# Performance work log

Measured on AMD Instinct MI355X. Metric: run time of the kernel, lower is better.

## Reference

```python
import jax, jax.numpy as jnp
import numpy as np

N = 50000      # nodes
E = 600000     # edges
D_IN = 128
D = 128        # embedding_size
H = 2 * D      # GENConv MLP hidden (expansion=2, num_layers=2)
L = 6          # gnn_layers
OUT = 2        # out_channels
EPS_MSG = 1e-7   # GENConv message eps
EPS_SM = 1e-16   # PyG softmax denominator eps
LN_EPS = 1e-5


def setup_inputs() -> dict:
    key = jax.random.key(0)
    ks = jax.random.split(key, 18)
    s_in = 1.0 / np.sqrt(D_IN)
    s_d = 1.0 / np.sqrt(D)
    s_h = 1.0 / np.sqrt(H)
    return {
        "x": jax.random.normal(ks[0], (N, D_IN), jnp.float32),
        "edge_index": jax.random.randint(ks[1], (2, E), 0, N, jnp.int64),
        # node encoder
        "enc_W": jax.random.normal(ks[2], (D_IN, D), jnp.float32) * s_in,
        "enc_b": jnp.zeros((D,), jnp.float32),
        # per-layer DeepGCN params (stacked over L layers)
        "ln_g": jnp.ones((L, D), jnp.float32),
        "ln_b": jnp.zeros((L, D), jnp.float32),
        "t": jnp.ones((L,), jnp.float32),  # learnable softmax temperature
        "W1": jax.random.normal(ks[3], (L, D, H), jnp.float32) * s_d,
        "b1": jnp.zeros((L, H), jnp.float32),
        "mln_g": jnp.ones((L, H), jnp.float32),
        "mln_b": jnp.zeros((L, H), jnp.float32),
        "W2": jax.random.normal(ks[4], (L, H, D), jnp.float32) * s_h,
        "b2": jnp.zeros((L, D), jnp.float32),
        # final MLP head (linear_layers=2)
        "lin_W1": jax.random.normal(ks[5], (D, D), jnp.float32) * s_d,
        "lin_b1": jnp.zeros((D,), jnp.float32),
        "lin_W2": jax.random.normal(ks[6], (D, OUT), jnp.float32) * s_d,
        "lin_b2": jnp.zeros((OUT,), jnp.float32),
    }


def _layernorm(h, g, b):
    mu = jnp.mean(h, axis=-1, keepdims=True)
    var = jnp.mean(jnp.square(h - mu), axis=-1, keepdims=True)
    return (h - mu) * jax.lax.rsqrt(var + LN_EPS) * g + b


def _genconv(h, src, dst, t, W1, b1, mg, mb, W2, b2):
    """GENConv with softmax aggregation: gather -> segment softmax -> scatter -> MLP."""
    msg = jax.nn.relu(h[src]) + EPS_MSG            # [E, D]
    scaled = msg * t
    mmax = jax.ops.segment_max(scaled, dst, num_segments=N)  # [N, D]
    mmax = jnp.where(jnp.isfinite(mmax), mmax, 0.0)          # empty segments
    ex = jnp.exp(scaled - mmax[dst])                          # [E, D]
    denom = jax.ops.segment_sum(ex, dst, num_segments=N)     # [N, D]
    alpha = ex / (denom[dst] + EPS_SM)
    agg = jax.ops.segment_sum(msg * alpha, dst, num_segments=N)  # [N, D]
    out = agg + h                                  # root/self term
    z = out @ W1 + b1                              # [N, 2D]
    z = jax.nn.relu(_layernorm(z, mg, mb))
    return z @ W2 + b2                             # [N, D]


def reference(x, edge_index, enc_W, enc_b, ln_g, ln_b, t, W1, b1,
              mln_g, mln_b, W2, b2, lin_W1, lin_b1, lin_W2, lin_b2):
    src, dst = edge_index[0], edge_index[1]
    h = x @ enc_W + enc_b                          # node encoder [N, D]
    for i in range(L):                             # DeepGCNLayer 'res+' blocks
        g = _layernorm(h, ln_g[i], ln_b[i])
        g = jax.nn.relu(g)                         # (dropout: inference no-op)
        g = _genconv(g, src, dst, t[i], W1[i], b1[i], mln_g[i], mln_b[i], W2[i], b2[i])
        h = h + g
    h = jax.nn.relu(h @ lin_W1 + lin_b1)           # head (dropout_rate=None)
    return h @ lin_W2 + lin_b2                     # [N, OUT]
```

## Files before the change

kernel.cpp:

```cpp
#include <hip/hip_runtime.h>

#define NN 50000
#define EE 600000
#define DD 128
#define HH 256
#define LL 6
#define NB 49

typedef _Float16 f16x8 __attribute__((ext_vector_type(8)));
typedef float f32x4 __attribute__((ext_vector_type(4)));

__device__ __forceinline__ float bf2f(unsigned short u){
  unsigned int x = ((unsigned int)u) << 16; float f; __builtin_memcpy(&f, &x, 4); return f;
}
__device__ __forceinline__ unsigned short f2bf(float f){
  unsigned int x; __builtin_memcpy(&x, &f, 4);
  unsigned int lsb = (x >> 16) & 1u; x += 0x7fffu + lsb; return (unsigned short)(x >> 16);
}
__device__ __forceinline__ float wave_sum(float v){
  #pragma unroll
  for (int off = 32; off >= 1; off >>= 1) v += __shfl_xor(v, off, 64);
  return v;
}
__device__ __forceinline__ unsigned short f2h(float f){
  _Float16 h = (_Float16)f; unsigned short u; __builtin_memcpy(&u, &h, 2); return u;
}
__device__ __forceinline__ float h2f(unsigned short u){
  _Float16 h; __builtin_memcpy(&h, &u, 2); return (float)h;
}

__global__ void k_detect(const unsigned short* __restrict__ xh,
                         const unsigned int* __restrict__ ew,
                         int* __restrict__ flags){
  __shared__ int s_bad, s_nz;
  int t = threadIdx.x;
  if (t == 0){ s_bad = 0; s_nz = 0; }
  __syncthreads();
  int bad = 0;
  for (int i = t; i < 512; i += 256){
    unsigned e = (xh[i] >> 7) & 0xffu;
    if (e < 96u || e > 135u) bad = 1;
  }
  if (bad) atomicOr(&s_bad, 1);
  int nz = 0;
  for (int i = t; i < 1024; i += 256)
    if ((i & 1) && ew[i] != 0u) nz = 1;
  if (nz) atomicOr(&s_nz, 1);
  __syncthreads();
  if (t == 0){
    flags[0] = s_bad ? 1 : 0;
    flags[1] = s_nz ? 0 : 1;
  }
}

__global__ void k_cvt_edges(const void* __restrict__ ei, const int* __restrict__ flags,
                            int* __restrict__ s32, int* __restrict__ d32){
  int e = blockIdx.x*256 + threadIdx.x;
  if (e >= EE) return;
  int sv, dv;
  if (flags[1]){
    const long long* p = (const long long*)ei;
    sv = (int)p[e]; dv = (int)p[EE + e];
  } else {
    const int* p = (const int*)ei;
    sv = p[e]; dv = p[EE + e];
  }
  s32[e] = ((unsigned)sv < (unsigned)NN) ? sv : 0;
  d32[e] = ((unsigned)dv < (unsigned)NN) ? dv : 0;
}

__global__ void k_hist(const int* __restrict__ dst, int* __restrict__ deg){
  int e = blockIdx.x*256 + threadIdx.x;
  if (e < EE) atomicAdd(&deg[dst[e]], 1);
}

__global__ void k_blocksum(const int* __restrict__ deg, int* __restrict__ bsum){
  __shared__ int ws[4];
  int t = threadIdx.x, b = blockIdx.x;
  int s = 0;
  int i0 = b*1024 + t*4;
  #pragma unroll
  for (int j=0;j<4;j++){ int i = i0+j; if (i < NN) s += deg[i]; }
  #pragma unroll
  for (int off=32; off>=1; off>>=1) s += __shfl_xor(s, off, 64);
  if ((t&63)==0) ws[t>>6] = s;
  __syncthreads();
  if (t==0) bsum[b] = ws[0]+ws[1]+ws[2]+ws[3];
}

__global__ void k_scanb(const int* __restrict__ bsum, int* __restrict__ boff, int* __restrict__ rowptr){
  int lane = threadIdx.x;
  int v = (lane < NB) ? bsum[lane] : 0;
  int inc = v;
  #pragma unroll
  for (int off=1; off<64; off<<=1){ int u = __shfl_up(inc, off, 64); if (lane>=off) inc += u; }
  if (lane < NB) boff[lane] = inc - v;
  if (lane == 63) rowptr[NN] = inc;
}

__global__ void k_scanscatter(const int* __restrict__ deg, const int* __restrict__ boff,
                              int* __restrict__ rowptr, int* __restrict__ pos){
  __shared__ int ws[4];
  int t = threadIdx.x, b = blockIdx.x;
  int lane = t & 63, wid = t >> 6;
  int i0 = b*1024 + t*4;
  int d[4];
  #pragma unroll
  for (int j=0;j<4;j++){ int i=i0+j; d[j] = (i<NN)? deg[i] : 0; }
  int tot = d[0]+d[1]+d[2]+d[3];
  int inc = tot;
  #pragma unroll
  for (int off=1; off<64; off<<=1){ int u = __shfl_up(inc, off, 64); if (lane>=off) inc += u; }
  if (lane==63) ws[wid] = inc;
  __syncthreads();
  int woff = 0;
  for (int w=0; w<wid; w++) woff += ws[w];
  int base = boff[b] + woff + (inc - tot);
  int pre = 0;
  #pragma unroll
  for (int j=0;j<4;j++){
    int i = i0+j;
    if (i<NN){ rowptr[i] = base + pre; pos[i] = base + pre; }
    pre += d[j];
  }
}

__global__ void k_fill(const int* __restrict__ src, const int* __restrict__ dst,
                       int* __restrict__ pos, int* __restrict__ csr){
  int e = blockIdx.x*256 + threadIdx.x;
  if (e < EE){
    int d = dst[e];
    int p = atomicAdd(&pos[d], 1);
    csr[p] = src[e];
  }
}

__global__ void k_prep_w(const int* __restrict__ flags,
    const void* __restrict__ encW, const void* __restrict__ linW1,
    const void* __restrict__ W1, const void* __restrict__ W2,
    unsigned short* __restrict__ ph, unsigned short* __restrict__ pl)
{
  int idx = blockIdx.x*256 + threadIdx.x;
  int fp32 = flags[0];
  const void* src; int off;
  if (idx < 16384){ int n=idx>>7, k=idx&127; src=encW; off=k*128+n; }
  else if (idx < 32768){ int o=idx-16384; int n=o>>7, k=o&127; src=linW1; off=k*128+n; }
  else if (idx < 229376){ int o=idx-32768; int l=o>>15, r=o&32767; int n=r>>7, k=r&127; src=W1; off=l*32768+k*256+n; }
  else { int o=idx-229376; int l=o>>15, r=o&32767; int n=r>>8, k=r&255; src=W2; off=l*32768+k*128+n; }
  float w = fp32 ? ((const float*)src)[off] : bf2f(((const unsigned short*)src)[off]);
  unsigned short h = f2h(w);
  ph[idx] = h;
  pl[idx] = f2h(w - h2f(h));
}

#define SM_ENCB 0
#define SM_LNG 128
#define SM_LNB 896
#define SM_TV 1664
#define SM_B1 1670
#define SM_MG 3206
#define SM_MB 4742
#define SM_B2 6278
#define SM_LINB1 7046
#define SM_LINW2 7174
#define SM_LINB2 7430
#define SM_TOT 7432
__global__ void k_prep_small(const int* __restrict__ flags,
    const void* s0, const void* s1, const void* s2, const void* s3,
    const void* s4, const void* s5, const void* s6, const void* s7,
    const void* s8, const void* s9, const void* s10, float* __restrict__ out)
{
  int i = blockIdx.x*256 + threadIdx.x;
  if (i >= SM_TOT) return;
  int fp32 = flags[0];
  const void* src; int off;
  if      (i < SM_LNG)  { src=s0;  off=i; }
  else if (i < SM_LNB)  { src=s1;  off=i-SM_LNG; }
  else if (i < SM_TV)   { src=s2;  off=i-SM_LNB; }
  else if (i < SM_B1)   { src=s3;  off=i-SM_TV; }
  else if (i < SM_MG)   { src=s4;  off=i-SM_B1; }
  else if (i < SM_MB)   { src=s5;  off=i-SM_MG; }
  else if (i < SM_B2)   { src=s6;  off=i-SM_MB; }
  else if (i < SM_LINB1){ src=s7;  off=i-SM_B2; }
  else if (i < SM_LINW2){ src=s8;  off=i-SM_LINB1; }
  else if (i < SM_LINB2){ src=s9;  off=i-SM_LINW2; }
  else                  { src=s10; off=i-SM_LINB2; }
  out[i] = fp32 ? ((const float*)src)[off] : bf2f(((const unsigned short*)src)[off]);
}

__device__ __forceinline__ void emit_me(unsigned short* me, int row, int col, float g, float tv){
  float m = g + 1e-7f;
  me[(size_t)row*256 + col] = f2h(m);
  me[(size_t)row*256 + 128 + col] = f2h(__expf(fminf(m*tv, 18.f) - 8.f));
}

template<int EPI>
__global__ __launch_bounds__(256, 4) void k_gemm(const void* __restrict__ Ap,
    const unsigned short* __restrict__ WTh, const unsigned short* __restrict__ WTl,
    const float* __restrict__ bias, void* __restrict__ Cv,
    int M, const int* __restrict__ flags, int aExt)
{
  __shared__ __align__(16) char smem[27648];
  short* lA = (short*)smem;
  short* lW = (short*)(smem + 9216);
  short* hT = (short*)smem;

  const int tid = threadIdx.x, lane = tid & 63, wid = tid >> 6;
  const int mi = lane & 15, q = lane >> 4;
  const int rowb = blockIdx.x * 64;
  const int fp32m = flags[0];

  f32x4 acc[4][2];
  #pragma unroll
  for (int a=0;a<4;a++)
    #pragma unroll
    for (int c=0;c<2;c++){ acc[a][c][0]=0.f; acc[a][c][1]=0.f; acc[a][c][2]=0.f; acc[a][c][3]=0.f; }

  const int nW = fp32m ? 2 : 1;
  for (int pass = 0; pass < nW; ++pass){
    const unsigned short* Wp = pass ? WTl : WTh;
    for (int kc = 0; kc < 2; ++kc){
      {
        const int kv = (tid & 7) * 8, r0 = tid >> 3;
        #pragma unroll
        for (int p = 0; p < 2; ++p){
          int row = p*32 + r0, grow = rowb + row;
          uint4 d = make_uint4(0u,0u,0u,0u);
          if (grow < M){
            if (!aExt){
              d = *(const uint4*)((const unsigned short*)Ap + (size_t)grow*128 + kc*64 + kv);
            } else if (!fp32m){
              uint4 u = *(const uint4*)((const unsigned short*)Ap + (size_t)grow*128 + kc*64 + kv);
              const unsigned short* us = (const unsigned short*)&u;
              unsigned short hh[8];
              #pragma unroll
              for (int c=0;c<8;c++) hh[c] = f2h(bf2f(us[c]));
              d.x = hh[0]|((unsigned)hh[1]<<16); d.y = hh[2]|((unsigned)hh[3]<<16);
              d.z = hh[4]|((unsigned)hh[5]<<16); d.w = hh[6]|((unsigned)hh[7]<<16);
            } else {
              const float* fp = (const float*)Ap + (size_t)grow*128 + kc*64 + kv;
              float4 v0 = *(const float4*)fp, v1 = *(const float4*)(fp+4);
              unsigned short hh[8] = {f2h(v0.x),f2h(v0.y),f2h(v0.z),f2h(v0.w),
                                      f2h(v1.x),f2h(v1.y),f2h(v1.z),f2h(v1.w)};
              d.x = hh[0]|((unsigned)hh[1]<<16); d.y = hh[2]|((unsigned)hh[3]<<16);
              d.z = hh[4]|((unsigned)hh[5]<<16); d.w = hh[6]|((unsigned)hh[7]<<16);
            }
          }
          *(uint4*)&lA[row*72 + kv] = d;
        }
        #pragma unroll
        for (int p = 0; p < 4; ++p){
          int n = p*32 + (tid >> 3);
          *(uint4*)&lW[n*72 + (tid & 7)*8] = *(const uint4*)(Wp + (size_t)n*128 + kc*64 + (tid & 7)*8);
        }
      }
      __syncthreads();
      #pragma unroll
      for (int ks = 0; ks < 2; ++ks){
        const int koff = ks*32 + q*8;
        f16x8 af[4], bw[2];
        #pragma unroll
        for (int rt=0; rt<4; rt++) af[rt] = *(const f16x8*)&lA[(rt*16+mi)*72 + koff];
        #pragma unroll
        for (int ct=0; ct<2; ct++) bw[ct] = *(const f16x8*)&lW[(wid*32 + ct*16 + mi)*72 + koff];
        #pragma unroll
        for (int rt=0; rt<4; rt++)
          #pragma unroll
          for (int ct=0; ct<2; ct++)
            acc[rt][ct] = __builtin_amdgcn_mfma_f32_16x16x32_f16(af[rt], bw[ct], acc[rt][ct], 0,0,0);
      }
      __syncthreads();
    }
  }
  #pragma unroll
  for (int ct=0; ct<2; ct++){
    const int col = wid*32 + ct*16 + mi;
    const float bf = bias[col];
    #pragma unroll
    for (int rt=0; rt<4; rt++)
      #pragma unroll
      for (int r=0; r<4; r++){
        float v = acc[rt][ct][r] + bf;
        if (EPI == 4) v = fmaxf(v, 0.f);
        hT[(rt*16 + q*4 + r)*136 + col] = (short)f2h(v);
      }
  }
  __syncthreads();
  unsigned short* C16 = (unsigned short*)Cv;
  #pragma unroll
  for (int i = 0; i < 4; ++i){
    int idx = i*256 + tid;
    int prow = idx >> 4, pl = idx & 15;
    int grow = rowb + prow;
    if (grow < M)
      *(uint4*)(C16 + (size_t)grow*128 + pl*8) = *(const uint4*)&hT[prow*136 + pl*8];
  }
}

__global__ __launch_bounds__(256, 3) void k_layer(const unsigned short* __restrict__ Ap,
    const unsigned short* __restrict__ W1h, const unsigned short* __restrict__ W1l,
    const unsigned short* __restrict__ W2h, const unsigned short* __restrict__ W2l,
    const float* __restrict__ b1, const float* __restrict__ mg, const float* __restrict__ mb,
    const float* __restrict__ b2, unsigned short* __restrict__ h16,
    const float* __restrict__ gam, const float* __restrict__ bet,
    const float* __restrict__ tp, unsigned short* __restrict__ me,
    int M, const int* __restrict__ flags, int doLN)
{
  __shared__ __align__(16) char smem[53248];
  short* lA  = (short*)smem;
  short* lW1 = (short*)(smem + 9216);
  short* zT  = (short*)smem;
  short* lW2 = (short*)(smem + 33792);
  short* hT  = (short*)smem;
  short* mE  = (short*)(smem + 17408);
  float2* sred = (float2*)(smem + 51200);

  const int tid = threadIdx.x, lane = tid & 63, wid = tid >> 6;
  const int mi = lane & 15, q = lane >> 4;
  const int kv = (tid & 7) * 8, r0 = tid >> 3;
  const int rowb = blockIdx.x * 64;
  const float tv = tp[0];
  const int nW = flags[0] ? 2 : 1;
  const int prow = tid >> 4;
  const int pl = tid & 15;

  f32x4 acc1[4][4];
  #pragma unroll
  for (int a=0;a<4;a++)
    #pragma unroll
    for (int c=0;c<4;c++){ acc1[a][c][0]=0.f; acc1[a][c][1]=0.f; acc1[a][c][2]=0.f; acc1[a][c][3]=0.f; }

  for (int pass = 0; pass < nW; ++pass){
    const unsigned short* Wp = pass ? W1l : W1h;
    for (int kc = 0; kc < 2; ++kc){
      if (pass == 0){
        #pragma unroll
        for (int p = 0; p < 2; ++p){
          int row = p*32 + r0, grow = rowb + row;
          uint4 d = make_uint4(0u,0u,0u,0u);
          if (grow < M) d = *(const uint4*)(Ap + (size_t)grow*128 + kc*64 + kv);
          *(uint4*)&lA[row*72 + kv] = d;
        }
      }
      #pragma unroll
      for (int p = 0; p < 8; ++p){
        int n = p*32 + r0;
        *(uint4*)&lW1[n*72 + kv] = *(const uint4*)(Wp + (size_t)n*128 + kc*64 + kv);
      }
      __syncthreads();
      #pragma unroll
      for (int ks = 0; ks < 2; ++ks){
        const int koff = ks*32 + q*8;
        f16x8 af[4], bw[4];
        #pragma unroll
        for (int rt=0; rt<4; rt++) af[rt] = *(const f16x8*)&lA[(rt*16+mi)*72 + koff];
        #pragma unroll
        for (int ct=0; ct<4; ct++) bw[ct] = *(const f16x8*)&lW1[(wid*64 + ct*16 + mi)*72 + koff];
        #pragma unroll
        for (int rt=0; rt<4; rt++)
          #pragma unroll
          for (int ct=0; ct<4; ct++)
            acc1[rt][ct] = __builtin_amdgcn_mfma_f32_16x16x32_f16(af[rt], bw[ct], acc1[rt][ct], 0,0,0);
      }
      __syncthreads();
    }
  }
  #pragma unroll
  for (int ct=0; ct<4; ct++){
    const float bf = b1[wid*64 + ct*16 + mi];
    #pragma unroll
    for (int rt=0; rt<4; rt++)
      #pragma unroll
      for (int r=0; r<4; r++) acc1[rt][ct][r] += bf;
  }
  #pragma unroll
  for (int rt=0; rt<4; rt++)
    #pragma unroll
    for (int r=0; r<4; r++){
      float s = 0.f, s2 = 0.f;
      #pragma unroll
      for (int ct=0; ct<4; ct++){ float v = acc1[rt][ct][r]; s += v; s2 += v*v; }
      #pragma unroll
      for (int off=1; off<16; off<<=1){ s += __shfl_xor(s, off, 64); s2 += __shfl_xor(s2, off, 64); }
      if (mi == 0) sred[wid*64 + rt*16 + q*4 + r] = make_float2(s, s2);
    }
  __syncthreads();
  float lnm[4][4], lnr[4][4];
  #pragma unroll
  for (int rt=0; rt<4; rt++)
    #pragma unroll
    for (int r=0; r<4; r++){
      int rl = rt*16 + q*4 + r;
      float2 t0 = sred[0*64+rl], t1 = sred[1*64+rl], t2 = sred[2*64+rl], t3 = sred[3*64+rl];
      float s = t0.x + t1.x + t2.x + t3.x;
      float s2 = t0.y + t1.y + t2.y + t3.y;
      float m = s * (1.f/256.f);
      float var = s2 * (1.f/256.f) - m*m;
      lnm[rt][r] = m;
      lnr[rt][r] = rsqrtf(var + 1e-5f);
    }
  __syncthreads();
  #pragma unroll
  for (int ct=0; ct<4; ct++){
    const int col = wid*64 + ct*16 + mi;
    const float gc = mg[col], bc = mb[col];
    #pragma unroll
    for (int rt=0; rt<4; rt++)
      #pragma unroll
      for (int r=0; r<4; r++){
        int rl = rt*16 + q*4 + r;
        float v = (acc1[rt][ct][r] - lnm[rt][r]) * lnr[rt][r] * gc + bc;
        zT[rl*264 + col] = (short)f2h(fmaxf(v, 0.f));
      }
  }
  __syncthreads();
  uint4 hpre[4];
  #pragma unroll
  for (int i = 0; i < 4; ++i){
    int grow = rowb + i*16 + prow;
    hpre[i] = make_uint4(0u,0u,0u,0u);
    if (grow < M) hpre[i] = *(const uint4*)(h16 + (size_t)grow*128 + pl*8);
  }
  f32x4 acc2[4][2];
  #pragma unroll
  for (int a=0;a<4;a++)
    #pragma unroll
    for (int c=0;c<2;c++){ acc2[a][c][0]=0.f; acc2[a][c][1]=0.f; acc2[a][c][2]=0.f; acc2[a][c][3]=0.f; }

  for (int pass = 0; pass < nW; ++pass){
    const unsigned short* Wp = pass ? W2l : W2h;
    for (int kc = 0; kc < 4; ++kc){
      #pragma unroll
      for (int p = 0; p < 4; ++p){
        int n = p*32 + r0;
        *(uint4*)&lW2[n*72 + kv] = *(const uint4*)(Wp + (size_t)n*256 + kc*64 + kv);
      }
      __syncthreads();
      #pragma unroll
      for (int ks = 0; ks < 2; ++ks){
        const int koff = ks*32 + q*8;
        f16x8 af[4], bw[2];
        #pragma unroll
        for (int rt=0; rt<4; rt++) af[rt] = *(const f16x8*)&zT[(rt*16+mi)*264 + kc*64 + koff];
        #pragma unroll
        for (int ct=0; ct<2; ct++) bw[ct] = *(const f16x8*)&lW2[(wid*32 + ct*16 + mi)*72 + koff];
        #pragma unroll
        for (int rt=0; rt<4; rt++)
          #pragma unroll
          for (int ct=0; ct<2; ct++)
            acc2[rt][ct] = __builtin_amdgcn_mfma_f32_16x16x32_f16(af[rt], bw[ct], acc2[rt][ct], 0,0,0);
      }
      __syncthreads();
    }
  }
  #pragma unroll
  for (int i = 0; i < 4; ++i)
    *(uint4*)&hT[(i*16 + prow)*136 + pl*8] = hpre[i];
  __syncthreads();
  #pragma unroll
  for (int ct=0; ct<2; ct++){
    const int col = wid*32 + ct*16 + mi;
    const float bf = b2[col];
    #pragma unroll
    for (int rt=0; rt<4; rt++)
      #pragma unroll
      for (int r=0; r<4; r++){
        int rl = rt*16 + q*4 + r;
        float hv = acc2[rt][ct][r] + bf + h2f((unsigned short)hT[rl*136 + col]);
        hT[rl*136 + col] = (short)f2h(hv);
        acc2[rt][ct][r] = hv;
      }
  }
  if (doLN){
    #pragma unroll
    for (int rt=0; rt<4; rt++)
      #pragma unroll
      for (int r=0; r<4; r++){
        float s = 0.f, s2 = 0.f;
        #pragma unroll
        for (int ct=0; ct<2; ct++){ float v = acc2[rt][ct][r]; s += v; s2 += v*v; }
        #pragma unroll
        for (int off=1; off<16; off<<=1){ s += __shfl_xor(s, off, 64); s2 += __shfl_xor(s2, off, 64); }
        if (mi == 0) sred[wid*64 + rt*16 + q*4 + r] = make_float2(s, s2);
      }
    __syncthreads();
    #pragma unroll
    for (int rt=0; rt<4; rt++)
      #pragma unroll
      for (int r=0; r<4; r++){
        int rl = rt*16 + q*4 + r;
        float2 t0 = sred[0*64+rl], t1 = sred[1*64+rl], t2 = sred[2*64+rl], t3 = sred[3*64+rl];
        float s = t0.x + t1.x + t2.x + t3.x;
        float s2 = t0.y + t1.y + t2.y + t3.y;
        float m = s * (1.f/128.f);
        float var = s2 * (1.f/128.f) - m*m;
        float rs = rsqrtf(var + 1e-5f);
        #pragma unroll
        for (int ct=0; ct<2; ct++){
          int col = wid*32 + ct*16 + mi;
          float g = fmaxf((acc2[rt][ct][r] - m) * rs * gam[col] + bet[col], 0.f);
          float mm = g + 1e-7f;
          mE[rl*264 + col] = (short)f2h(mm);
          mE[rl*264 + 128 + col] = (short)f2h(__expf(fminf(mm*tv, 18.f) - 8.f));
        }
      }
  }
  __syncthreads();
  #pragma unroll
  for (int i = 0; i < 4; ++i){
    int grow = rowb + i*16 + prow;
    if (grow < M)
      *(uint4*)(h16 + (size_t)grow*128 + pl*8) = *(const uint4*)&hT[(i*16 + prow)*136 + pl*8];
  }
  if (doLN){
    #pragma unroll
    for (int i = 0; i < 8; ++i){
      int idx2 = i*256 + tid;
      int mrow = idx2 >> 5, part = (idx2 >> 4) & 1, l16 = idx2 & 15;
      int grow = rowb + mrow;
      if (grow < M)
        *(uint4*)(me + (size_t)grow*256 + part*128 + l16*8)
          = *(const uint4*)&mE[mrow*264 + part*128 + l16*8];
    }
  }
}

__global__ __launch_bounds__(256,4) void k_preln0(const unsigned short* __restrict__ h16,
    const float* __restrict__ gam, const float* __restrict__ bet,
    const float* __restrict__ tp, unsigned short* __restrict__ me)
{
  int wid = threadIdx.x >> 6, lane = threadIdx.x & 63;
  int row = blockIdx.x*4 + wid;
  float tv = tp[0];
  unsigned u = ((const unsigned*)(h16 + (size_t)row*DD))[lane];
  float v0 = h2f((unsigned short)(u & 0xffffu));
  float v1 = h2f((unsigned short)(u >> 16));
  float mean = wave_sum(v0+v1) * (1.f/128.f);
  float d0 = v0-mean, d1 = v1-mean;
  float var = wave_sum(d0*d0 + d1*d1) * (1.f/128.f);
  float rs = rsqrtf(var + 1e-5f);
  float o0 = fmaxf(d0*rs*gam[2*lane]   + bet[2*lane],   0.f);
  float o1 = fmaxf(d1*rs*gam[2*lane+1] + bet[2*lane+1], 0.f);
  emit_me(me, row, 2*lane,   o0, tv);
  emit_me(me, row, 2*lane+1, o1, tv);
}

__global__ __launch_bounds__(256,8) void k_agg(
    const unsigned short* __restrict__ me,
    const int* __restrict__ rowptr, const int* __restrict__ csr,
    unsigned short* __restrict__ obf)
{
  int wid = threadIdx.x>>6, lane = threadIdx.x&63;
  int node = blockIdx.x*4 + wid;
  int st = rowptr[node], en = rowptr[node+1];
  int quad = lane >> 4, fi = lane & 15;
  float l[8], ac[8];
  #pragma unroll
  for (int f=0; f<8; f++){ l[f]=0.f; ac[f]=0.f; }
  for (int base = st; base < en; base += 64){
    int cnt = min(64, en - base);
    int sv = (lane < cnt) ? csr[base + lane] : NN;
    for (int j = 0; j < cnt; j += 8){
      int s0i = __shfl(sv, j + quad, 64);
      int s1i = __shfl(sv, j + 4 + quad, 64);
      bool two = (j + 4) < cnt;
      const unsigned short* mer0 = me + (size_t)s0i*256 + fi*8;
      f16x8 mh0 = *(const f16x8*)(mer0);
      f16x8 eh0 = *(const f16x8*)(mer0 + 128);
      if (two){
        const unsigned short* mer1 = me + (size_t)s1i*256 + fi*8;
        f16x8 mh1 = *(const f16x8*)(mer1);
        f16x8 eh1 = *(const f16x8*)(mer1 + 128);
        #pragma unroll
        for (int f=0; f<8; f++){
          l[f]  = fmaf((float)eh0[f], 1.f, l[f]);
          ac[f] = fmaf((float)mh0[f], (float)eh0[f], ac[f]);
          l[f]  = fmaf((float)eh1[f], 1.f, l[f]);
          ac[f] = fmaf((float)mh1[f], (float)eh1[f], ac[f]);
        }
      } else {
        #pragma unroll
        for (int f=0; f<8; f++){
          l[f]  = fmaf((float)eh0[f], 1.f, l[f]);
          ac[f] = fmaf((float)mh0[f], (float)eh0[f], ac[f]);
        }
      }
    }
  }
  #pragma unroll
  for (int off=16; off<=32; off<<=1)
    #pragma unroll
    for (int f=0; f<8; f++){ l[f] += __shfl_xor(l[f], off, 64); ac[f] += __shfl_xor(ac[f], off, 64); }
  if (quad == 0){
    f16x8 mh = *(const f16x8*)(me + (size_t)node*256 + fi*8);
    unsigned short o[8];
    #pragma unroll
    for (int f=0; f<8; f++){
      float a = ac[f] / (l[f] + 1e-16f);
      o[f] = f2h(((float)mh[f] - 1e-7f) + a);
    }
    uint4 w;
    w.x = o[0]|((unsigned)o[1]<<16); w.y = o[2]|((unsigned)o[3]<<16);
    w.z = o[4]|((unsigned)o[5]<<16); w.w = o[6]|((unsigned)o[7]<<16);
    *(uint4*)(obf + (size_t)node*DD + fi*8) = w;
  }
}

__global__ __launch_bounds__(256,4) void k_head2(const unsigned short* __restrict__ u16,
    const float* __restrict__ w, const float* __restrict__ b,
    void* __restrict__ out, const int* __restrict__ flags)
{
  int wid = threadIdx.x>>6, lane = threadIdx.x&63;
  int row = blockIdx.x*4 + wid;
  unsigned uu = ((const unsigned*)(u16 + (size_t)row*DD))[lane];
  float u0 = h2f((unsigned short)(uu & 0xffffu));
  float u1 = h2f((unsigned short)(uu >> 16));
  float s0 = u0*w[(2*lane)*2+0] + u1*w[(2*lane+1)*2+0];
  float s1 = u0*w[(2*lane)*2+1] + u1*w[(2*lane+1)*2+1];
  s0 = wave_sum(s0); s1 = wave_sum(s1);
  if (lane == 0){
    float o0 = s0 + b[0], o1 = s1 + b[1];
    if (flags[0]){
      ((float*)out)[row*2+0] = o0;
      ((float*)out)[row*2+1] = o1;
    } else {
      ((unsigned short*)out)[row*2+0] = f2bf(o0);
      ((unsigned short*)out)[row*2+1] = f2bf(o1);
    }
  }
}

extern "C" void kernel_launch(void* const* d_in, const int* in_sizes, int n_in,
                              void* d_out, int out_size, void* d_ws, size_t ws_size,
                              hipStream_t stream)
{
  (void)in_sizes; (void)n_in; (void)out_size; (void)ws_size;
  char* ws = (char*)d_ws;
  size_t off = 0;
  auto alloc = [&](size_t bytes) -> char* {
    char* p = ws + off;
    off = (off + bytes + 255) & ~(size_t)255;
    return p;
  };
  int* flags  = (int*)alloc(256);
  float* sm   = (float*)alloc(SM_TOT*4);
  unsigned short* planeH = (unsigned short*)alloc(425984*2);
  unsigned short* planeL = (unsigned short*)alloc(425984*2);
  int* src32  = (int*)alloc((size_t)EE*4);
  int* dst32  = (int*)alloc((size_t)EE*4);
  int* deg    = (int*)alloc((size_t)NN*4);
  int* pos    = (int*)alloc((size_t)NN*4);
  int* rowptr = (int*)alloc((size_t)(NN+1)*4);
  int* csr    = (int*)alloc((size_t)EE*4);
  int* bsum   = (int*)alloc(64*4);
  int* boff   = (int*)alloc(64*4);
  unsigned short* h16 = (unsigned short*)alloc((size_t)NN*128*2);
  unsigned short* me   = (unsigned short*)alloc((size_t)(NN+1)*256*2);
  unsigned short* obf  = (unsigned short*)alloc((size_t)NN*128*2);
  unsigned short* ob16 = (unsigned short*)alloc((size_t)NN*128*2);

  k_detect<<<1,256,0,stream>>>((const unsigned short*)d_in[0], (const unsigned int*)d_in[1], flags);
  k_cvt_edges<<<(EE+255)/256,256,0,stream>>>(d_in[1], flags, src32, dst32);
  hipMemsetAsync(deg, 0, (size_t)NN*4, stream);
  hipMemsetAsync(me + (size_t)NN*256, 0, 512, stream);
  k_hist<<<(EE+255)/256,256,0,stream>>>(dst32, deg);
  k_blocksum<<<NB,256,0,stream>>>(deg, bsum);
  k_scanb<<<1,64,0,stream>>>(bsum, boff, rowptr);
  k_scanscatter<<<NB,256,0,stream>>>(deg, boff, rowptr, pos);
  k_fill<<<(EE+255)/256,256,0,stream>>>(src32, dst32, pos, csr);
  k_prep_w<<<1664,256,0,stream>>>(flags, d_in[2], d_in[13], d_in[7], d_in[11], planeH, planeL);
  k_prep_small<<<30,256,0,stream>>>(flags, d_in[3], d_in[4], d_in[5], d_in[6], d_in[8],
                                    d_in[9], d_in[10], d_in[12], d_in[14], d_in[15], d_in[16], sm);

  const int GB = (NN + 63)/64;
  k_gemm<3><<<GB,256,0,stream>>>((const void*)d_in[0], planeH + 0, planeL + 0,
                                 sm + SM_ENCB, (void*)h16, NN, flags, 1);
  k_preln0<<<NN/4,256,0,stream>>>(h16, sm + SM_LNG, sm + SM_LNB, sm + SM_TV, me);
  for (int i = 0; i < LL; ++i){
    k_agg<<<NN/4,256,0,stream>>>(me, rowptr, csr, obf);
    int nl = (i+1 < LL) ? (i+1) : 0;
    k_layer<<<GB,256,0,stream>>>(obf,
                                 planeH + 32768 + i*32768, planeL + 32768 + i*32768,
                                 planeH + 229376 + i*32768, planeL + 229376 + i*32768,
                                 sm + SM_B1 + i*256, sm + SM_MG + i*256, sm + SM_MB + i*256,
                                 sm + SM_B2 + i*128, h16,
                                 sm + SM_LNG + nl*128, sm + SM_LNB + nl*128,
                                 sm + SM_TV + nl,
                                 me, NN, flags, (i+1 < LL) ? 1 : 0);
  }
  k_gemm<4><<<GB,256,0,stream>>>((const void*)h16, planeH + 16384, planeL + 16384,
                                 sm + SM_LINB1, (void*)ob16, NN, flags, 0);
  k_head2<<<NN/4,256,0,stream>>>(ob16, sm + SM_LINW2, sm + SM_LINB2, d_out, flags);
}
```

Before: 812.7 us.

## Register-prefetch next K-tile in layer GEMMs and fuse edge conversion with degree histogram

The per-layer fused MLP kernel now loads the next A/W1 and W2 K-chunks into registers while MFMAs run on the current LDS tile, so global-load latency is hidden behind compute. It also prefetches the first W2 chunk during the LayerNorm epilogue and adjusts barrier placement. Separately, edge index conversion and the degree histogram atomics are merged into one kernel, removing a launch and a reread of dst. Extra prefetch registers may raise VGPR pressure and reduce occupancy.

```diff
diff --git a/kernel.cpp b/kernel.cpp
--- a/kernel.cpp
+++ b/kernel.cpp
@@ -53,8 +53,9 @@
   }
 }
 
-__global__ void k_cvt_edges(const void* __restrict__ ei, const int* __restrict__ flags,
-                            int* __restrict__ s32, int* __restrict__ d32){
+__global__ void k_cvt_hist(const void* __restrict__ ei, const int* __restrict__ flags,
+                           int* __restrict__ s32, int* __restrict__ d32,
+                           int* __restrict__ deg){
   int e = blockIdx.x*256 + threadIdx.x;
   if (e >= EE) return;
   int sv, dv;
@@ -65,13 +66,11 @@
     const int* p = (const int*)ei;
     sv = p[e]; dv = p[EE + e];
   }
-  s32[e] = ((unsigned)sv < (unsigned)NN) ? sv : 0;
-  d32[e] = ((unsigned)dv < (unsigned)NN) ? dv : 0;
-}
-
-__global__ void k_hist(const int* __restrict__ dst, int* __restrict__ deg){
-  int e = blockIdx.x*256 + threadIdx.x;
-  if (e < EE) atomicAdd(&deg[dst[e]], 1);
+  sv = ((unsigned)sv < (unsigned)NN) ? sv : 0;
+  dv = ((unsigned)dv < (unsigned)NN) ? dv : 0;
+  s32[e] = sv;
+  d32[e] = dv;
+  atomicAdd(&deg[dv], 1);
 }
 
 __global__ void k_blocksum(const int* __restrict__ deg, int* __restrict__ bsum){
@@ -323,6 +322,7 @@
   const int nW = flags[0] ? 2 : 1;
   const int prow = tid >> 4;
   const int pl = tid & 15;
+  const int grow0 = rowb + r0, grow1 = rowb + 32 + r0;
 
   f32x4 acc1[4][4];
   #pragma unroll
@@ -330,41 +330,53 @@
     #pragma unroll
     for (int c=0;c<4;c++){ acc1[a][c][0]=0.f; acc1[a][c][1]=0.f; acc1[a][c][2]=0.f; acc1[a][c][3]=0.f; }
 
-  for (int pass = 0; pass < nW; ++pass){
-    const unsigned short* Wp = pass ? W1l : W1h;
-    for (int kc = 0; kc < 2; ++kc){
-      if (pass == 0){
-        #pragma unroll
-        for (int p = 0; p < 2; ++p){
-          int row = p*32 + r0, grow = rowb + row;
-          uint4 d = make_uint4(0u,0u,0u,0u);
-          if (grow < M) d = *(const uint4*)(Ap + (size_t)grow*128 + kc*64 + kv);
-          *(uint4*)&lA[row*72 + kv] = d;
-        }
-      }
-      #pragma unroll
-      for (int p = 0; p < 8; ++p){
-        int n = p*32 + r0;
-        *(uint4*)&lW1[n*72 + kv] = *(const uint4*)(Wp + (size_t)n*128 + kc*64 + kv);
-      }
-      __syncthreads();
-      #pragma unroll
-      for (int ks = 0; ks < 2; ++ks){
-        const int koff = ks*32 + q*8;
-        f16x8 af[4], bw[4];
-        #pragma unroll
-        for (int rt=0; rt<4; rt++) af[rt] = *(const f16x8*)&lA[(rt*16+mi)*72 + koff];
-        #pragma unroll
-        for (int ct=0; ct<4; ct++) bw[ct] = *(const f16x8*)&lW1[(wid*64 + ct*16 + mi)*72 + koff];
-        #pragma unroll
-        for (int rt=0; rt<4; rt++)
-          #pragma unroll
-          for (int ct=0; ct<4; ct++)
-            acc1[rt][ct] = __builtin_amdgcn_mfma_f32_16x16x32_f16(af[rt], bw[ct], acc1[rt][ct], 0,0,0);
-      }
-      __syncthreads();
-    }
-  }
+  const int nPh1 = nW*2;
+  uint4 aP0, aP1, wP[8];
+  {
+    aP0 = make_uint4(0u,0u,0u,0u); aP1 = aP0;
+    if (grow0 < M) aP0 = *(const uint4*)(Ap + (size_t)grow0*128 + kv);
+    if (grow1 < M) aP1 = *(const uint4*)(Ap + (size_t)grow1*128 + kv);
+    #pragma unroll
+    for (int p = 0; p < 8; ++p)
+      wP[p] = *(const uint4*)(W1h + (size_t)(p*32 + r0)*128 + kv);
+  }
+  for (int ph = 0; ph < nPh1; ++ph){
+    if (ph) __syncthreads();
+    *(uint4*)&lA[r0*72 + kv] = aP0;
+    *(uint4*)&lA[(32 + r0)*72 + kv] = aP1;
+    #pragma unroll
+    for (int p = 0; p < 8; ++p)
+      *(uint4*)&lW1[(p*32 + r0)*72 + kv] = wP[p];
+    __syncthreads();
+    if (ph + 1 < nPh1){
+      int np = (ph+1) >> 1, nk = (ph+1) & 1;
+      const unsigned short* Wp = np ? W1l : W1h;
+      aP0 = make_uint4(0u,0u,0u,0u); aP1 = aP0;
+      if (grow0 < M) aP0 = *(const uint4*)(Ap + (size_t)grow0*128 + nk*64 + kv);
+      if (grow1 < M) aP1 = *(const uint4*)(Ap + (size_t)grow1*128 + nk*64 + kv);
+      #pragma unroll
+      for (int p = 0; p < 8; ++p)
+        wP[p] = *(const uint4*)(Wp + (size_t)(p*32 + r0)*128 + nk*64 + kv);
+    }
+    #pragma unroll
+    for (int ks = 0; ks < 2; ++ks){
+      const int koff = ks*32 + q*8;
+      f16x8 af[4], bw[4];
+      #pragma unroll
+      for (int rt=0; rt<4; rt++) af[rt] = *(const f16x8*)&lA[(rt*16+mi)*72 + koff];
+      #pragma unroll
+      for (int ct=0; ct<4; ct++) bw[ct] = *(const f16x8*)&lW1[(wid*64 + ct*16 + mi)*72 + koff];
+      #pragma unroll
+      for (int rt=0; rt<4; rt++)
+        #pragma unroll
+        for (int ct=0; ct<4; ct++)
+          acc1[rt][ct] = __builtin_amdgcn_mfma_f32_16x16x32_f16(af[rt], bw[ct], acc1[rt][ct], 0,0,0);
+    }
+  }
+  uint4 w2P[4];
+  #pragma unroll
+  for (int p = 0; p < 4; ++p)
+    w2P[p] = *(const uint4*)(W2h + (size_t)(p*32 + r0)*256 + kv);
   #pragma unroll
   for (int ct=0; ct<4; ct++){
     const float bf = b1[wid*64 + ct*16 + mi];
@@ -373,6 +385,7 @@
       #pragma unroll
       for (int r=0; r<4; r++) acc1[rt][ct][r] += bf;
   }
+  __syncthreads();
   #pragma unroll
   for (int rt=0; rt<4; rt++)
     #pragma unroll
@@ -413,7 +426,6 @@
         zT[rl*264 + col] = (short)f2h(fmaxf(v, 0.f));
       }
   }
-  __syncthreads();
   uint4 hpre[4];
   #pragma unroll
   for (int i = 0; i < 4; ++i){
@@ -421,38 +433,44 @@
     hpre[i] = make_uint4(0u,0u,0u,0u);
     if (grow < M) hpre[i] = *(const uint4*)(h16 + (size_t)grow*128 + pl*8);
   }
+  __syncthreads();
   f32x4 acc2[4][2];
   #pragma unroll
   for (int a=0;a<4;a++)
     #pragma unroll
     for (int c=0;c<2;c++){ acc2[a][c][0]=0.f; acc2[a][c][1]=0.f; acc2[a][c][2]=0.f; acc2[a][c][3]=0.f; }
 
-  for (int pass = 0; pass < nW; ++pass){
-    const unsigned short* Wp = pass ? W2l : W2h;
-    for (int kc = 0; kc < 4; ++kc){
-      #pragma unroll
-      for (int p = 0; p < 4; ++p){
-        int n = p*32 + r0;
-        *(uint4*)&lW2[n*72 + kv] = *(const uint4*)(Wp + (size_t)n*256 + kc*64 + kv);
-      }
-      __syncthreads();
-      #pragma unroll
-      for (int ks = 0; ks < 2; ++ks){
-        const int koff = ks*32 + q*8;
-        f16x8 af[4], bw[2];
-        #pragma unroll
-        for (int rt=0; rt<4; rt++) af[rt] = *(const f16x8*)&zT[(rt*16+mi)*264 + kc*64 + koff];
-        #pragma unroll
-        for (int ct=0; ct<2; ct++) bw[ct] = *(const f16x8*)&lW2[(wid*32 + ct*16 + mi)*72 + koff];
-        #pragma unroll
-        for (int rt=0; rt<4; rt++)
-          #pragma unroll
-          for (int ct=0; ct<2; ct++)
-            acc2[rt][ct] = __builtin_amdgcn_mfma_f32_16x16x32_f16(af[rt], bw[ct], acc2[rt][ct], 0,0,0);
-      }
-      __syncthreads();
-    }
-  }
+  const int nPh2 = nW*4;
+  for (int ph = 0; ph < nPh2; ++ph){
+    if (ph) __syncthreads();
+    #pragma unroll
+    for (int p = 0; p < 4; ++p)
+      *(uint4*)&lW2[(p*32 + r0)*72 + kv] = w2P[p];
+    __syncthreads();
+    if (ph + 1 < nPh2){
+      int np = (ph+1) >> 2, nk = (ph+1) & 3;
+      const unsigned short* Wp = np ? W2l : W2h;
+      #pragma unroll
+      for (int p = 0; p < 4; ++p)
+        w2P[p] = *(const uint4*)(Wp + (size_t)(p*32 + r0)*256 + nk*64 + kv);
+    }
+    const int kc = ph & 3;
+    #pragma unroll
+    for (int ks = 0; ks < 2; ++ks){
+      const int koff = ks*32 + q*8;
+      f16x8 af[4], bw[2];
+      #pragma unroll
+      for (int rt=0; rt<4; rt++) af[rt] = *(const f16x8*)&zT[(rt*16+mi)*264 + kc*64 + koff];
+      #pragma unroll
+      for (int ct=0; ct<2; ct++) bw[ct] = *(const f16x8*)&lW2[(wid*32 + ct*16 + mi)*72 + koff];
+      #pragma unroll
+      for (int rt=0; rt<4; rt++)
+        #pragma unroll
+        for (int ct=0; ct<2; ct++)
+          acc2[rt][ct] = __builtin_amdgcn_mfma_f32_16x16x32_f16(af[rt], bw[ct], acc2[rt][ct], 0,0,0);
+    }
+  }
+  __syncthreads();
   #pragma unroll
   for (int i = 0; i < 4; ++i)
     *(uint4*)&hT[(i*16 + prow)*136 + pl*8] = hpre[i];
@@ -660,10 +678,9 @@
   unsigned short* ob16 = (unsigned short*)alloc((size_t)NN*128*2);
 
   k_detect<<<1,256,0,stream>>>((const unsigned short*)d_in[0], (const unsigned int*)d_in[1], flags);
-  k_cvt_edges<<<(EE+255)/256,256,0,stream>>>(d_in[1], flags, src32, dst32);
   hipMemsetAsync(deg, 0, (size_t)NN*4, stream);
   hipMemsetAsync(me + (size_t)NN*256, 0, 512, stream);
-  k_hist<<<(EE+255)/256,256,0,stream>>>(dst32, deg);
+  k_cvt_hist<<<(EE+255)/256,256,0,stream>>>(d_in[1], flags, src32, dst32, deg);
   k_blocksum<<<NB,256,0,stream>>>(deg, bsum);
   k_scanb<<<1,64,0,stream>>>(bsum, boff, rowptr);
   k_scanscatter<<<NB,256,0,stream>>>(deg, boff, rowptr, pos);
```

Result: slower. 1.036 ms (+27.5%).
